# Performance work log

Measured on AMD Instinct MI355X. Metric: run time of the kernel, lower is better.

## Reference

```python
import jax, jax.numpy as jnp
import numpy as np

# Static module config (from Encoder's CropConv layers)
B, CIN, COUT, H, W = 32, 256, 256, 64, 64
K, STRIDE, PAD, DIL = 3, 2, 1, 1
OVERLAP, CENTER = 0, 4


def _build_crop_mask(in_h, out_h, out_w, center_size, overlap):
    """Faithful replica of CropConv's python-loop mask construction,
    including python-slice clamping to L = out_h*out_w."""
    L = out_h * out_w
    crop_start = (in_h - in_h // center_size) // 2 - overlap
    start_idx = in_h * crop_start + crop_start
    crop_size = in_h // center_size + overlap * 2
    not_cropped = crop_start * 2

    def seg_len(a, b):
        # length of python slice [a:b] on an array of length L
        return max(0, min(b, L) - min(a, L))

    segs = []
    for i in range(crop_size):
        if i == 0:
            segs.append(np.ones(seg_len(0, start_idx), bool))
        if i == crop_size - 1:
            segs.append(np.zeros(seg_len(start_idx, start_idx + crop_size), bool))
            segs.append(np.ones(seg_len(start_idx + crop_size, in_h * in_h), bool))
            break
        segs.append(np.zeros(seg_len(start_idx, start_idx + crop_size), bool))
        segs.append(np.ones(seg_len(start_idx + crop_size, start_idx + not_cropped), bool))
        start_idx += in_h
    mask = np.concatenate(segs)
    assert mask.shape[0] == L, (mask.shape[0], L)
    return mask.reshape(out_h, out_w)


def setup_inputs() -> dict:
    key = jax.random.key(0)
    kx, kw = jax.random.split(key)
    x = jax.random.normal(kx, (B, CIN, H, W), dtype=jnp.float32)
    # kaiming_normal(mode='fan_out', nonlinearity='relu'): std = sqrt(2 / (COUT*K*K))
    std = np.sqrt(2.0 / (COUT * K * K)).astype(np.float32)
    weight = jax.random.normal(kw, (COUT, CIN, K, K), dtype=jnp.float32) * std
    return {"x": x, "weight": weight}


def reference(x, weight):
    out_h = (H - K + 2 * PAD) // STRIDE + 1
    out_w = (W - K + 2 * PAD) // STRIDE + 1
    # unfold + matmul == standard convolution; use the efficient fused form
    out = jax.lax.conv_general_dilated(
        x, weight,
        window_strides=(STRIDE, STRIDE),
        padding=[(PAD, PAD), (PAD, PAD)],
        rhs_dilation=(DIL, DIL),
        dimension_numbers=("NCHW", "OIHW", "NCHW"))  # [B, COUT, out_h, out_w]
    mask = jnp.asarray(_build_crop_mask(H, out_h, out_w, CENTER, OVERLAP))
    return jnp.where(mask[None, None, :, :], out, jnp.float32(0.0))
```

## Files before the change

kernel.cpp:

```cpp
#include <hip/hip_runtime.h>


#define B_   32
#define CIN  256
#define COUT 256
#define H_   64
#define W_   64
#define OH   32
#define OW   32

typedef _Float16 f16;
typedef _Float16 half8 __attribute__((ext_vector_type(8)));
typedef float    floatx16 __attribute__((ext_vector_type(16)));

__global__ __launch_bounds__(256) void repack_w_kernel(const float* __restrict__ w,
                                                       f16* __restrict__ rp) {
  int o = blockIdx.x * 256 + threadIdx.x;
  int ci_l = o & 15;
  int tt = o >> 4;
  int co_l = tt & 127; tt >>= 7;
  int khw = tt % 9;    tt /= 9;
  int cc   = tt & 15;  tt >>= 4;
  int co_t = tt;
  int co = co_t * 128 + co_l;
  int ci = cc * 16 + ci_l;
  rp[o] = (f16)w[(co * CIN + ci) * 9 + khw];
}

static __device__ __forceinline__ void wg_barrier() {
  __builtin_amdgcn_sched_barrier(0);
  asm volatile("s_waitcnt lgkmcnt(0)" ::: "memory");
  __builtin_amdgcn_s_barrier();
  __builtin_amdgcn_sched_barrier(0);
}

__global__ __launch_bounds__(256, 2) void conv_mfma_kernel(
    const float* __restrict__ x, const f16* __restrict__ rp,
    float* __restrict__ out) {
  __shared__ __align__(16) f16 ws[18432];
  __shared__ __align__(16) f16 xs[19040];

  const int t    = threadIdx.x;
  const int lane = t & 63;
  const int wave = t >> 6;
  const int wm   = wave >> 1;
  const int wn   = wave & 1;

  const int blk  = blockIdx.x;
  const int b    = blk >> 4;
  const int rem  = blk & 15;
  const int co_t = rem >> 3;
  const int oh0  = (rem & 7) << 2;
  const int ih0  = 2 * oh0 - 1;

  const float* xb  = x + (size_t)b * CIN * H_ * W_;
  const f16*   rpb = rp + (size_t)co_t * (16 * 9 * 128 * 16);

  const int iw  = t & 63;
  const int rru = __builtin_amdgcn_readfirstlane(t >> 6);
  const int k0  = (lane >> 5) * 8;
  const int ml  = lane & 31;
  const int p_st   = iw & 1;
  const int idx_st = (iw + p_st) >> 1;
  const int gx     = (idx_st >> 3) & 1;

  f16* const xs0 = xs;
  f16* const xs1 = xs + 9520;

  floatx16 acc[2][2];
#pragma unroll
  for (int mi = 0; mi < 2; ++mi)
#pragma unroll
    for (int nj = 0; nj < 2; ++nj)
#pragma unroll
      for (int i = 0; i < 16; ++i) acc[mi][nj][i] = 0.f;

  float xva[3][2][8], xvb[3][2][8];
  half8 wv[9];

  auto load_x = [&](float (&xv)[3][2][8], int cc) {
    const float* bcc = xb + (size_t)cc * 16 * 4096;
#pragma unroll
    for (int it = 0; it < 3; ++it) {
      const int r = rru + it * 4;
      if (r < 9) {
        const int ih = ih0 + r;
        if (ih >= 0) {
          const float* p0 = bcc + (size_t)ih * 64 + iw;
#pragma unroll
          for (int g = 0; g < 2; ++g)
#pragma unroll
            for (int c = 0; c < 8; ++c)
              xv[it][g][c] = p0[(size_t)(g * 8 + c) * 4096];
        } else {
#pragma unroll
          for (int g = 0; g < 2; ++g)
#pragma unroll
            for (int c = 0; c < 8; ++c) xv[it][g][c] = 0.f;
        }
      }
    }
  };

  auto load_w = [&](int cc) {
    const half8* src = (const half8*)(rpb + (size_t)cc * 18432);
#pragma unroll
    for (int i = 0; i < 9; ++i) wv[i] = src[t + i * 256];
  };

  auto write_x = [&](float (&xv)[3][2][8], f16* xoth) {
    f16* d = xoth + p_st * 4760 + idx_st * 16;
#pragma unroll
    for (int it = 0; it < 3; ++it) {
      const int r = rru + it * 4;
      if (r < 9) {
#pragma unroll
        for (int g = 0; g < 2; ++g) {
          half8 v;
#pragma unroll
          for (int c = 0; c < 8; ++c) v[c] = (f16)xv[it][g][c];
          *(half8*)&d[r * 528 + (g ^ gx) * 8] = v;
        }
      }
    }
  };

  const int colw = (t >> 1) & 127;
  f16* const wdst = ws + colw * 16 + (((t & 1) * 8) ^ (colw & 8));
  auto write_w = [&]() {
#pragma unroll
    for (int i = 0; i < 9; ++i) *(half8*)&wdst[i * 2048] = wv[i];
  };

  const f16* const Aw = ws + wm * 1024 + ml * 16 + (k0 ^ (ml & 8));

  auto compute = [&](const f16* xcur) {
    const f16* Be  = xcur + wn * 2112 + ml * 16 + (k0 ^ (ml & 8));
    const f16* Bo1 = Be + 4760;
    const f16* Bo2 = xcur + 4760 + wn * 2112 + (ml + 1) * 16 + (k0 ^ ((ml + 1) & 8));
    __builtin_amdgcn_s_setprio(1);
#pragma unroll
    for (int kh = 0; kh < 3; ++kh) {
#pragma unroll
      for (int kw = 0; kw < 3; ++kw) {
        const int khw = kh * 3 + kw;
        half8 a0 = *(const half8*)&Aw[khw * 2048];
        half8 a1 = *(const half8*)&Aw[khw * 2048 + 512];
        const f16* Bp = (kw == 0) ? Bo1 : (kw == 1) ? Be : Bo2;
#pragma unroll
        for (int nj = 0; nj < 2; ++nj) {
          half8 bf = *(const half8*)&Bp[nj * 1056 + kh * 528];
          acc[0][nj] = __builtin_amdgcn_mfma_f32_32x32x16_f16(a0, bf, acc[0][nj], 0, 0, 0);
          acc[1][nj] = __builtin_amdgcn_mfma_f32_32x32x16_f16(a1, bf, acc[1][nj], 0, 0, 0);
        }
      }
    }
    __builtin_amdgcn_s_setprio(0);
  };

  if (t < 144) {
    const int r = t >> 4, ci = t & 15;
    xs0[4760 + r * 528 + ci] = (f16)0.f;
    xs1[4760 + r * 528 + ci] = (f16)0.f;
  }

  load_x(xva, 0); load_w(0);
  write_x(xva, xs0);
  write_w();
  load_x(xva, 1);
  load_x(xvb, 2);
  load_w(1);
  __syncthreads();

#pragma unroll 1
  for (int cc = 0; cc < 16; cc += 2) {
    compute(xs0);
    write_x(xva, xs1);
    if (cc + 3 < 16) load_x(xva, cc + 3);
    wg_barrier();
    write_w();
    if (cc + 2 < 16) load_w(cc + 2);
    wg_barrier();

    compute(xs1);
    if (cc + 2 < 16) write_x(xvb, xs0);
    if (cc + 4 < 16) load_x(xvb, cc + 4);
    wg_barrier();
    if (cc + 2 < 16) write_w();
    if (cc + 3 < 16) load_w(cc + 3);
    wg_barrier();
  }

  const int col = ml;
  const int rowbase = (lane >> 5) * 4;
  float* ob = out + ((size_t)b * COUT + co_t * 128 + wm * 64) * (OH * OW);
#pragma unroll
  for (int mi = 0; mi < 2; ++mi) {
#pragma unroll
    for (int nj = 0; nj < 2; ++nj) {
      const int oh = oh0 + wn * 2 + nj;
#pragma unroll
      for (int r = 0; r < 16; ++r) {
        const int row = mi * 32 + (r & 3) + 8 * (r >> 2) + rowbase;
        ob[(size_t)row * (OH * OW) + oh * OW + col] = acc[mi][nj][r];
      }
    }
  }
}

extern "C" void kernel_launch(void* const* d_in, const int* in_sizes, int n_in,
                              void* d_out, int out_size, void* d_ws, size_t ws_size,
                              hipStream_t stream) {
  const float* x = (const float*)d_in[0];
  const float* w = (const float*)d_in[1];
  float* out = (float*)d_out;
  f16* rp = (f16*)d_ws;

  repack_w_kernel<<<2304, 256, 0, stream>>>(w, rp);
  conv_mfma_kernel<<<512, 256, 0, stream>>>(x, rp, out);
}
```

Baseline: 225.1 us.

## Load conv weight fragments directly from global memory instead of staging in LDS

Weight A-fragments are now read straight from the repacked global buffer into registers for each of the 9 taps, and the LDS weight buffer and its write/barrier phase are removed. The loop is simplified to a single x double buffer with one barrier per channel chunk and a single-stage register prefetch of x. This cuts LDS traffic, LDS footprint and half the barriers, but each wave now issues uncoalesced-ish global loads for weights at the start of every compute, with no prefetch ahead of use. That exposes global latency, and the shallower x prefetch (one chunk ahead instead of two) leaves less time to hide load latency.

Result: no change. 227.9 us (+1.3%).

```diff
diff --git a/kernel.cpp b/kernel.cpp
--- a/kernel.cpp
+++ b/kernel.cpp
@@ -37,7 +37,6 @@
 __global__ __launch_bounds__(256, 2) void conv_mfma_kernel(
     const float* __restrict__ x, const f16* __restrict__ rp,
     float* __restrict__ out) {
-  __shared__ __align__(16) f16 ws[18432];
   __shared__ __align__(16) f16 xs[19040];
 
   const int t    = threadIdx.x;
@@ -53,8 +52,7 @@
   const int oh0  = (rem & 7) << 2;
   const int ih0  = 2 * oh0 - 1;
 
-  const float* xb  = x + (size_t)b * CIN * H_ * W_;
-  const f16*   rpb = rp + (size_t)co_t * (16 * 9 * 128 * 16);
+  const float* xb = x + (size_t)b * CIN * H_ * W_;
 
   const int iw  = t & 63;
   const int rru = __builtin_amdgcn_readfirstlane(t >> 6);
@@ -67,6 +65,9 @@
   f16* const xs0 = xs;
   f16* const xs1 = xs + 9520;
 
+  const f16* const AbL = rp + (size_t)co_t * (16 * 9 * 128 * 16)
+                            + (wm * 64 + ml) * 16 + k0;
+
   floatx16 acc[2][2];
 #pragma unroll
   for (int mi = 0; mi < 2; ++mi)
@@ -75,11 +76,9 @@
 #pragma unroll
       for (int i = 0; i < 16; ++i) acc[mi][nj][i] = 0.f;
 
-  float xva[3][2][8], xvb[3][2][8];
-  half8 wv[9];
-
-  auto load_x = [&](float (&xv)[3][2][8], int cc) {
-    const float* bcc = xb + (size_t)cc * 16 * 4096;
+  float xv[3][2][8];
+
+  auto load_x = [&](const float* bcc) {
 #pragma unroll
     for (int it = 0; it < 3; ++it) {
       const int r = rru + it * 4;
@@ -102,13 +101,7 @@
     }
   };
 
-  auto load_w = [&](int cc) {
-    const half8* src = (const half8*)(rpb + (size_t)cc * 18432);
-#pragma unroll
-    for (int i = 0; i < 9; ++i) wv[i] = src[t + i * 256];
-  };
-
-  auto write_x = [&](float (&xv)[3][2][8], f16* xoth) {
+  auto write_x = [&](f16* xoth) {
     f16* d = xoth + p_st * 4760 + idx_st * 16;
 #pragma unroll
     for (int it = 0; it < 3; ++it) {
@@ -125,16 +118,13 @@
     }
   };
 
-  const int colw = (t >> 1) & 127;
-  f16* const wdst = ws + colw * 16 + (((t & 1) * 8) ^ (colw & 8));
-  auto write_w = [&]() {
-#pragma unroll
-    for (int i = 0; i < 9; ++i) *(half8*)&wdst[i * 2048] = wv[i];
-  };
-
-  const f16* const Aw = ws + wm * 1024 + ml * 16 + (k0 ^ (ml & 8));
-
-  auto compute = [&](const f16* xcur) {
+  auto compute = [&](const f16* Abc, const f16* xcur) {
+    half8 a0[9], a1[9];
+#pragma unroll
+    for (int khw = 0; khw < 9; ++khw) {
+      a0[khw] = *(const half8*)&Abc[khw * 2048];
+      a1[khw] = *(const half8*)&Abc[khw * 2048 + 512];
+    }
     const f16* Be  = xcur + wn * 2112 + ml * 16 + (k0 ^ (ml & 8));
     const f16* Bo1 = Be + 4760;
     const f16* Bo2 = xcur + 4760 + wn * 2112 + (ml + 1) * 16 + (k0 ^ ((ml + 1) & 8));
@@ -144,14 +134,12 @@
 #pragma unroll
       for (int kw = 0; kw < 3; ++kw) {
         const int khw = kh * 3 + kw;
-        half8 a0 = *(const half8*)&Aw[khw * 2048];
-        half8 a1 = *(const half8*)&Aw[khw * 2048 + 512];
         const f16* Bp = (kw == 0) ? Bo1 : (kw == 1) ? Be : Bo2;
 #pragma unroll
         for (int nj = 0; nj < 2; ++nj) {
           half8 bf = *(const half8*)&Bp[nj * 1056 + kh * 528];
-          acc[0][nj] = __builtin_amdgcn_mfma_f32_32x32x16_f16(a0, bf, acc[0][nj], 0, 0, 0);
-          acc[1][nj] = __builtin_amdgcn_mfma_f32_32x32x16_f16(a1, bf, acc[1][nj], 0, 0, 0);
+          acc[0][nj] = __builtin_amdgcn_mfma_f32_32x32x16_f16(a0[khw], bf, acc[0][nj], 0, 0, 0);
+          acc[1][nj] = __builtin_amdgcn_mfma_f32_32x32x16_f16(a1[khw], bf, acc[1][nj], 0, 0, 0);
         }
       }
     }
@@ -164,31 +152,24 @@
     xs1[4760 + r * 528 + ci] = (f16)0.f;
   }
 
-  load_x(xva, 0); load_w(0);
-  write_x(xva, xs0);
-  write_w();
-  load_x(xva, 1);
-  load_x(xvb, 2);
-  load_w(1);
+  load_x(xb);
+  write_x(xs0);
+  load_x(xb + 65536);
   __syncthreads();
 
+  const f16* Abc = AbL;
+  f16* curp = xs0;
+  f16* othp = xs1;
 #pragma unroll 1
-  for (int cc = 0; cc < 16; cc += 2) {
-    compute(xs0);
-    write_x(xva, xs1);
-    if (cc + 3 < 16) load_x(xva, cc + 3);
-    wg_barrier();
-    write_w();
-    if (cc + 2 < 16) load_w(cc + 2);
-    wg_barrier();
-
-    compute(xs1);
-    if (cc + 2 < 16) write_x(xvb, xs0);
-    if (cc + 4 < 16) load_x(xvb, cc + 4);
-    wg_barrier();
-    if (cc + 2 < 16) write_w();
-    if (cc + 3 < 16) load_w(cc + 3);
-    wg_barrier();
+  for (int cc = 0; cc < 16; ++cc) {
+    compute(Abc, curp);
+    Abc += 18432;
+    if (cc < 15) {
+      write_x(othp);
+      if (cc < 14) load_x(xb + (size_t)(cc + 2) * 65536);
+      wg_barrier();
+      f16* tm = curp; curp = othp; othp = tm;
+    }
   }
 
   const int col = ml;
```
